# Kernel optimization log

Measured on AMD Instinct MI355X. Metric: run time of the kernel, lower is better.

Reference implementation:

```python
import jax, jax.numpy as jnp
import numpy as np

AXIAL_WEIGHT = 1.0
N_NODES = 1_000_000
N_ELEM = 2_000_000


def setup_inputs() -> dict:
    key = jax.random.key(0)
    ks = jax.random.split(key, 12)
    N, E = N_NODES, N_ELEM
    pred_raw = jax.random.normal(ks[0], (N, 3), jnp.float32)
    u_c = jax.random.uniform(ks[1], (1,), jnp.float32) + 0.5
    theta_c = jax.random.uniform(ks[2], (1,), jnp.float32) + 0.5
    connectivity = jax.random.randint(ks[3], (E, 2), 0, N, jnp.int32)
    # lengths / section properties bounded away from zero (1/L^3 appears)
    elem_lengths = jax.random.uniform(ks[4], (E,), jnp.float32) + 0.5
    prop_E = jax.random.uniform(ks[5], (E,), jnp.float32) + 1.0
    prop_A = jax.random.uniform(ks[6], (E,), jnp.float32) + 0.5
    prop_I22 = jax.random.uniform(ks[7], (E,), jnp.float32) + 0.5
    ang = jax.random.uniform(ks[8], (E,), jnp.float32) * (2.0 * np.pi)
    # columns: [cos, 0, sin] -- forward reads cols 0 and 2
    elem_directions = jnp.stack([jnp.cos(ang), jnp.zeros_like(ang), jnp.sin(ang)], axis=1)
    F_ext = jax.random.normal(ks[9], (N, 3), jnp.float32)
    bc_disp = (jax.random.uniform(ks[10], (N, 1)) < 0.05).astype(jnp.float32)
    bc_rot = (jax.random.uniform(ks[11], (N, 1)) < 0.05).astype(jnp.float32)
    return {
        "pred_raw": pred_raw, "u_c": u_c, "theta_c": theta_c,
        "elem_lengths": elem_lengths, "prop_E": prop_E, "prop_A": prop_A,
        "prop_I22": prop_I22, "elem_directions": elem_directions,
        "F_ext": F_ext, "bc_disp": bc_disp, "bc_rot": bc_rot,
        "connectivity": connectivity,
    }


def reference(pred_raw, u_c, theta_c, elem_lengths, prop_E, prop_A, prop_I22,
              elem_directions, F_ext, bc_disp, bc_rot, connectivity):
    n_nodes = pred_raw.shape[0]
    # physical displacements: [ux*u_c, uz*u_c, th*theta_c]
    scale = jnp.concatenate([u_c, u_c, theta_c])  # [3]
    u_phys = pred_raw * scale[None, :]

    nA = connectivity[:, 0]
    nB = connectivity[:, 1]
    c = elem_directions[:, 0]
    s = elem_directions[:, 2]
    L = elem_lengths
    EA = prop_E * prop_A
    EI = prop_E * prop_I22

    uA = u_phys[nA]  # [E,3] gather
    uB = u_phys[nB]
    u_A = c * uA[:, 0] + s * uA[:, 1]
    w_A = -s * uA[:, 0] + c * uA[:, 1]
    th_A = -uA[:, 2]
    u_B = c * uB[:, 0] + s * uB[:, 1]
    w_B = -s * uB[:, 0] + c * uB[:, 1]
    th_B = -uB[:, 2]

    ea_l = EA / L * AXIAL_WEIGHT
    ei_l = EI / L
    ei_l2 = EI / L**2
    ei_l3 = EI / L**3

    # analytic K_loc @ d_local (K_loc is the standard 6x6 beam stiffness)
    dw = w_A - w_B
    f0 = ea_l * (u_A - u_B)
    f1 = 12.0 * ei_l3 * dw + 6.0 * ei_l2 * (th_A + th_B)
    f2 = 6.0 * ei_l2 * dw + 4.0 * ei_l * th_A + 2.0 * ei_l * th_B
    f3 = -f0
    f4 = -f1
    f5 = 6.0 * ei_l2 * dw + 2.0 * ei_l * th_A + 4.0 * ei_l * th_B

    fA = jnp.stack([c * f0 - s * f1, s * f0 + c * f1, -f2], axis=1)  # [E,3]
    fB = jnp.stack([c * f3 - s * f4, s * f3 + c * f4, -f5], axis=1)

    F_int = jax.ops.segment_sum(
        jnp.concatenate([fA, fB], axis=0),
        jnp.concatenate([nA, nB], axis=0),
        num_segments=n_nodes)  # [N,3] scatter-add

    R = F_int - F_ext
    free_mask = jnp.concatenate([1.0 - bc_disp, 1.0 - bc_disp, 1.0 - bc_rot], axis=1)
    R_free = R * free_mask
    F_free = F_ext * free_mask
    F_norm_sq = jnp.maximum(jnp.sum(F_free**2), 1e-30)
    loss = jnp.sum(R_free**2) / F_norm_sq  # single graph -> n_graphs = 1
    return loss
```

## Files before the change

### kernel.cpp

```cpp
#include <hip/hip_runtime.h>
#include <hip/hip_fp16.h>


#define SPANC  4096
#define NBC    256
#define CURP   16
#define FTH    1024
#define FBE    2048
#define ATH    1024
#define CB     96

struct F3 { float x, y, z; };

__device__ __forceinline__ uint2 packrec(float fx, float fy, float fz, int local) {
    unsigned short hx = __half_as_ushort(__float2half(fx));
    unsigned short hy = __half_as_ushort(__float2half(fy));
    unsigned short hz = __half_as_ushort(__float2half(fz));
    return make_uint2(((unsigned)hy << 16) | hx, ((unsigned)local << 16) | hz);
}

__device__ __forceinline__ int block_incl_scan(int v, int* wsum, int lane, int wv) {
    #pragma unroll
    for (int off = 1; off < 64; off <<= 1) {
        int t = __shfl_up(v, off, 64);
        if (lane >= off) v += t;
    }
    if (lane == 63) wsum[wv] = v;
    __syncthreads();
    if (wv == 0) {
        int w = (lane < 16) ? wsum[lane] : 0;
        #pragma unroll
        for (int off = 1; off < 16; off <<= 1) {
            int t = __shfl_up(w, off, 64);
            if (lane >= off) w += t;
        }
        if (lane < 16) wsum[lane] = w;
    }
    __syncthreads();
    return v + ((wv > 0) ? wsum[wv - 1] : 0);
}

__global__ void __launch_bounds__(1024)
count_kernel(const long long* __restrict__ conn, int* __restrict__ rows,
             int cs, int ce) {
    __shared__ int h[NBC];
    int tid = threadIdx.x;
    if (tid < NBC) h[tid] = 0;
    __syncthreads();
    int stride = gridDim.x * 1024;
    for (int e = cs + blockIdx.x * 1024 + tid; e < ce; e += stride) {
        long long v = __builtin_nontemporal_load(conn + e);
        int na = (int)(unsigned)((unsigned long long)v & 0xFFFFFFFFull);
        int nb = (int)(unsigned)((unsigned long long)v >> 32);
        atomicAdd(&h[na >> 12], 1);
        atomicAdd(&h[nb >> 12], 1);
    }
    __syncthreads();
    if (tid < NBC) rows[blockIdx.x * NBC + tid] = h[tid];
}

__global__ void __launch_bounds__(1024)
scan_kernel(const int* __restrict__ rows, int* __restrict__ cursor,
            int* __restrict__ base, double* __restrict__ accSlots,
            int isFirst) {
    __shared__ int wsum[16];
    int tid = threadIdx.x, lane = tid & 63, wv = tid >> 6;
    int c = 0;
    if (tid < NBC) {
        #pragma unroll 4
        for (int r = 0; r < CB; ++r) c += rows[r * NBC + tid];
    }
    int incl = block_incl_scan(c, wsum, lane, wv);
    if (tid < NBC) {
        base[tid + 1] = incl;
        cursor[tid * CURP] = incl - c;
    }
    if (tid == 0) base[0] = 0;
    if (isFirst && tid < 512) accSlots[tid] = 0.0;
}

__global__ void __launch_bounds__(1024)
fill_kernel(const long long* __restrict__ conn,
            const F3*  __restrict__ pred,
            const float* __restrict__ u_c,
            const float* __restrict__ theta_c,
            const float* __restrict__ len,
            const float* __restrict__ pE,
            const float* __restrict__ pA,
            const float* __restrict__ pI,
            const float* __restrict__ dir,
            uint2* __restrict__ arena,
            int* __restrict__ cursor,
            int cs, int ce) {
    __shared__ uint2         slab[2 * FBE];
    __shared__ unsigned char sbk [2 * FBE];
    __shared__ int hist [NBC];
    __shared__ int boff [NBC];
    __shared__ int astart[NBC];
    __shared__ int wsum [16];

    int tid = threadIdx.x, lane = tid & 63, wv = tid >> 6;

    if (tid < NBC) hist[tid] = 0;
    __syncthreads();

    float uc = u_c[0];
    float tc = theta_c[0];
    int bs = cs + blockIdx.x * FBE;
    int be = bs + FBE; if (be > ce) be = ce;

    unsigned sv[4];
    uint2    rc[4];

    #pragma unroll
    for (int j = 0; j < 2; ++j) {
        int e = bs + j * FTH + tid;
        unsigned sa = 0xFFFFFFFFu, sb = 0xFFFFFFFFu;
        if (e < be) {
            long long cv = __builtin_nontemporal_load(conn + e);
            int na = (int)(unsigned)((unsigned long long)cv & 0xFFFFFFFFull);
            int nb = (int)(unsigned)((unsigned long long)cv >> 32);

            F3 pa_ = pred[na];
            F3 pb_ = pred[nb];

            float c  = __builtin_nontemporal_load(&dir[3 * e + 0]);
            float s  = __builtin_nontemporal_load(&dir[3 * e + 2]);
            float L  = __builtin_nontemporal_load(&len[e]);
            float Ee = __builtin_nontemporal_load(&pE[e]);
            float EA = Ee * __builtin_nontemporal_load(&pA[e]);
            float EI = Ee * __builtin_nontemporal_load(&pI[e]);

            float a0 = pa_.x * uc;
            float a1 = pa_.y * uc;
            float a2 = pa_.z * tc;
            float b0 = pb_.x * uc;
            float b1 = pb_.y * uc;
            float b2 = pb_.z * tc;

            float u_A  =  c * a0 + s * a1;
            float w_A  = -s * a0 + c * a1;
            float th_A = -a2;
            float u_B  =  c * b0 + s * b1;
            float w_B  = -s * b0 + c * b1;
            float th_B = -b2;

            float invL  = 1.0f / L;
            float ea_l  = EA * invL;
            float ei_l  = EI * invL;
            float ei_l2 = ei_l  * invL;
            float ei_l3 = ei_l2 * invL;

            float dw = w_A - w_B;
            float f0 = ea_l * (u_A - u_B);
            float f1 = 12.0f * ei_l3 * dw + 6.0f * ei_l2 * (th_A + th_B);
            float f2 = 6.0f * ei_l2 * dw + 4.0f * ei_l * th_A + 2.0f * ei_l * th_B;
            float f5 = 6.0f * ei_l2 * dw + 2.0f * ei_l * th_A + 4.0f * ei_l * th_B;

            float fA0 = c * f0 - s * f1;
            float fA1 = s * f0 + c * f1;

            int bkA = na >> 12;
            int rA  = atomicAdd(&hist[bkA], 1);
            sa = ((unsigned)rA << 8) | (unsigned)bkA;
            rc[2 * j + 0] = packrec(fA0, fA1, -f2, na & 4095);

            int bkB = nb >> 12;
            int rB  = atomicAdd(&hist[bkB], 1);
            sb = ((unsigned)rB << 8) | (unsigned)bkB;
            rc[2 * j + 1] = packrec(-fA0, -fA1, -f5, nb & 4095);
        }
        sv[2 * j + 0] = sa;
        sv[2 * j + 1] = sb;
    }
    __syncthreads();

    int h = (tid < NBC) ? hist[tid] : 0;
    if (tid < NBC && h) astart[tid] = atomicAdd(&cursor[tid * CURP], h);
    int iT = block_incl_scan(h, wsum, lane, wv);
    if (tid < NBC) boff[tid] = iT - h;
    __syncthreads();

    #pragma unroll
    for (int r = 0; r < 4; ++r) {
        unsigned s2 = sv[r];
        if (s2 != 0xFFFFFFFFu) {
            int bk = (int)(s2 & 255u);
            int rk = (int)(s2 >> 8);
            int slot = boff[bk] + rk;
            slab[slot] = rc[r];
            sbk[slot]  = (unsigned char)bk;
        }
    }
    __syncthreads();

    int tot = boff[NBC - 1] + hist[NBC - 1];
    for (int i = tid; i < tot; i += FTH) {
        int bk = sbk[i];
        arena[astart[bk] + (i - boff[bk])] = slab[i];
    }
}

__global__ void __launch_bounds__(1024)
accum_kernel(const unsigned long long* __restrict__ arena,
             const int* __restrict__ base,
             const float* __restrict__ Fext,
             const float* __restrict__ bcd,
             const float* __restrict__ bcr,
             double* __restrict__ accSlots,
             float* __restrict__ fint32,
             __half* __restrict__ fint16,
             int N, int isFirst, int isLast, int mode) {
    __shared__ float tile[SPANC * 3];
    __shared__ double sn[16], sd[16];

    int tid = threadIdx.x, lane = tid & 63, wv = tid >> 6;
    int b = blockIdx.x;
    int nodeLo = b * SPANC;
    int gBase = nodeLo * 3;
    int gMax  = 3 * N;

    if (isFirst) {
        for (int i = tid; i < SPANC * 3; i += ATH) tile[i] = 0.0f;
    } else if (mode == 1) {
        for (int i = tid; i < SPANC * 3; i += ATH) {
            int g = gBase + i;
            tile[i] = (g < gMax) ? fint32[g] : 0.0f;
        }
    } else {
        for (int i = tid; i < SPANC * 3; i += ATH) {
            int g = gBase + i;
            tile[i] = (g < gMax) ? __half2float(fint16[g]) : 0.0f;
        }
    }
    __syncthreads();

    int s0 = base[b];
    int s1 = base[b + 1];
    for (int i = s0 + tid; i < s1; i += ATH) {
        unsigned long long rv = __builtin_nontemporal_load(arena + i);
        unsigned lo = (unsigned)(rv & 0xFFFFFFFFull);
        unsigned hi = (unsigned)(rv >> 32);
        float fx = __half2float(__ushort_as_half((unsigned short)(lo & 0xFFFFu)));
        float fy = __half2float(__ushort_as_half((unsigned short)(lo >> 16)));
        float fz = __half2float(__ushort_as_half((unsigned short)(hi & 0xFFFFu)));
        int local = (int)(hi >> 16);
        atomicAdd(&tile[local * 3 + 0], fx);
        atomicAdd(&tile[local * 3 + 1], fy);
        atomicAdd(&tile[local * 3 + 2], fz);
    }
    __syncthreads();

    if (!isLast) {
        if (mode == 1) {
            for (int i = tid; i < SPANC * 3; i += ATH) {
                int g = gBase + i;
                if (g < gMax) fint32[g] = tile[i];
            }
        } else {
            for (int i = tid; i < SPANC * 3; i += ATH) {
                int g = gBase + i;
                if (g < gMax) fint16[g] = __float2half(tile[i]);
            }
        }
        return;
    }

    int spanCnt = N - nodeLo;
    if (spanCnt > SPANC) spanCnt = SPANC;

    double num = 0.0, den = 0.0;
    for (int l = tid; l < spanCnt; l += ATH) {
        int n = nodeLo + l;
        float md = 1.0f - __builtin_nontemporal_load(&bcd[n]);
        float mr = 1.0f - __builtin_nontemporal_load(&bcr[n]);
        float e0 = __builtin_nontemporal_load(&Fext[3 * n + 0]);
        float e1 = __builtin_nontemporal_load(&Fext[3 * n + 1]);
        float e2 = __builtin_nontemporal_load(&Fext[3 * n + 2]);
        float r0 = (tile[l * 3 + 0] - e0) * md;
        float r1 = (tile[l * 3 + 1] - e1) * md;
        float r2 = (tile[l * 3 + 2] - e2) * mr;
        float g0 = e0 * md;
        float g1 = e1 * md;
        float g2 = e2 * mr;
        num += (double)r0 * r0 + (double)r1 * r1 + (double)r2 * r2;
        den += (double)g0 * g0 + (double)g1 * g1 + (double)g2 * g2;
    }
    #pragma unroll
    for (int off = 32; off > 0; off >>= 1) {
        num += __shfl_down(num, off, 64);
        den += __shfl_down(den, off, 64);
    }
    if (lane == 0) { sn[wv] = num; sd[wv] = den; }
    __syncthreads();
    if (tid == 0) {
        double tn = 0.0, td = 0.0;
        #pragma unroll
        for (int w = 0; w < 16; ++w) { tn += sn[w]; td += sd[w]; }
        double* slot = accSlots + (size_t)(b & 63) * 8;
        atomicAdd(&slot[0], tn);
        atomicAdd(&slot[1], td);
    }
}

__global__ void final_kernel(const double* __restrict__ accSlots,
                             float* __restrict__ out) {
    int t = threadIdx.x;
    double n = accSlots[t * 8 + 0];
    double d = accSlots[t * 8 + 1];
    #pragma unroll
    for (int off = 32; off > 0; off >>= 1) {
        n += __shfl_down(n, off, 64);
        d += __shfl_down(d, off, 64);
    }
    if (t == 0) {
        if (d < 1e-30) d = 1e-30;
        out[0] = (float)(n / d);
    }
}

static inline size_t align256(size_t x) { return (x + 255) & ~(size_t)255; }

extern "C" void kernel_launch(void* const* d_in, const int* in_sizes, int n_in,
                              void* d_out, int out_size, void* d_ws, size_t ws_size,
                              hipStream_t stream) {
    const F3*    pred    = (const F3*)d_in[0];
    const float* u_c     = (const float*)d_in[1];
    const float* theta_c = (const float*)d_in[2];
    const float* len     = (const float*)d_in[3];
    const float* pE      = (const float*)d_in[4];
    const float* pA      = (const float*)d_in[5];
    const float* pI      = (const float*)d_in[6];
    const float* dir     = (const float*)d_in[7];
    const float* Fext    = (const float*)d_in[8];
    const float* bcd     = (const float*)d_in[9];
    const float* bcr     = (const float*)d_in[10];
    const long long* conn = (const long long*)d_in[11];

    int N = in_sizes[0] / 3;
    int E = in_sizes[3];
    int NBc = (N + SPANC - 1) / SPANC;

    size_t oCur   = 4096;
    size_t oBase  = oCur + (size_t)NBC * CURP * 4;
    size_t oFint0 = align256(oBase + 4 * (NBC + 1));
    size_t rowsBytes = (size_t)CB * NBC * 4;

    const int cfgK[6] = {1, 2, 2, 4, 4, 8};
    const int cfgM[6] = {0, 1, 2, 1, 2, 2};
    int K = 8, mode = 2;
    size_t oF = oFint0, oA = oFint0;
    for (int t = 0; t < 6; ++t) {
        int Kc = cfgK[t], Mc = cfgM[t];
        size_t chunkE = (size_t)(E + Kc - 1) / Kc;
        size_t fsz = (Kc > 1) ? (size_t)3 * N * (Mc == 1 ? 4 : 2) : 0;
        size_t oAt = align256(oFint0 + fsz);
        size_t arenaB = 2 * chunkE * 8;
        if (arenaB < rowsBytes) arenaB = rowsBytes;
        size_t need = oAt + arenaB;
        if (need <= ws_size || t == 5) {
            K = Kc; mode = Mc; oF = oFint0; oA = oAt;
            if (need <= ws_size) break;
        }
    }

    int chunkElems = (E + K - 1) / K;

    double*             accSlots = (double*)d_ws;
    int*                cursor   = (int*)((char*)d_ws + oCur);
    int*                base     = (int*)((char*)d_ws + oBase);
    float*              fint32   = (float*)((char*)d_ws + oF);
    __half*             fint16   = (__half*)((char*)d_ws + oF);
    uint2*              arena    = (uint2*)((char*)d_ws + oA);
    unsigned long long* arenaLL  = (unsigned long long*)arena;
    int*                rows     = (int*)arena;

    for (int c = 0; c < K; ++c) {
        int cs = c * chunkElems;
        if (cs >= E) break;
        int ce = cs + chunkElems;
        if (ce > E) ce = E;
        int NT = (ce - cs + FBE - 1) / FBE;

        int isFirst = (c == 0);
        int isLast  = (ce == E);

        count_kernel<<<CB, 1024, 0, stream>>>(conn, rows, cs, ce);
        scan_kernel<<<1, 1024, 0, stream>>>(rows, cursor, base, accSlots, isFirst);
        fill_kernel<<<NT, FTH, 0, stream>>>(
            conn, pred, u_c, theta_c, len, pE, pA, pI, dir,
            arena, cursor, cs, ce);
        accum_kernel<<<NBc, ATH, 0, stream>>>(
            arenaLL, base, Fext, bcd, bcr, accSlots,
            fint32, fint16, N, isFirst, isLast, mode);
    }

    final_kernel<<<1, 64, 0, stream>>>(accSlots, (float*)d_out);
}
```

Baseline: 278.7 us.

## Prepack scaled node displacements to half, use nontemporal stores, retune chunk configs

```diff
diff --git a/kernel.cpp b/kernel.cpp
--- a/kernel.cpp
+++ b/kernel.cpp
@@ -41,6 +41,21 @@
 }
 
 __global__ void __launch_bounds__(1024)
+upack_kernel(const float* __restrict__ pred, const float* __restrict__ u_c,
+             const float* __restrict__ theta_c, uint2* __restrict__ up, int N) {
+    int i = blockIdx.x * 1024 + threadIdx.x;
+    if (i >= N) return;
+    float uc = u_c[0], tc = theta_c[0];
+    float x = __builtin_nontemporal_load(&pred[3 * i + 0]) * uc;
+    float y = __builtin_nontemporal_load(&pred[3 * i + 1]) * uc;
+    float z = __builtin_nontemporal_load(&pred[3 * i + 2]) * tc;
+    unsigned hx = __half_as_ushort(__float2half(x));
+    unsigned hy = __half_as_ushort(__float2half(y));
+    unsigned hz = __half_as_ushort(__float2half(z));
+    up[i] = make_uint2((hy << 16) | hx, hz);
+}
+
+__global__ void __launch_bounds__(1024)
 count_kernel(const long long* __restrict__ conn, int* __restrict__ rows,
              int cs, int ce) {
     __shared__ int h[NBC];
@@ -56,7 +71,8 @@
         atomicAdd(&h[nb >> 12], 1);
     }
     __syncthreads();
-    if (tid < NBC) rows[blockIdx.x * NBC + tid] = h[tid];
+    if (tid < NBC)
+        __builtin_nontemporal_store(h[tid], &rows[blockIdx.x * NBC + tid]);
 }
 
 __global__ void __launch_bounds__(1024)
@@ -81,9 +97,7 @@
 
 __global__ void __launch_bounds__(1024)
 fill_kernel(const long long* __restrict__ conn,
-            const F3*  __restrict__ pred,
-            const float* __restrict__ u_c,
-            const float* __restrict__ theta_c,
+            const uint2* __restrict__ upk,
             const float* __restrict__ len,
             const float* __restrict__ pE,
             const float* __restrict__ pA,
@@ -104,8 +118,6 @@
     if (tid < NBC) hist[tid] = 0;
     __syncthreads();
 
-    float uc = u_c[0];
-    float tc = theta_c[0];
     int bs = cs + blockIdx.x * FBE;
     int be = bs + FBE; if (be > ce) be = ce;
 
@@ -121,8 +133,8 @@
             int na = (int)(unsigned)((unsigned long long)cv & 0xFFFFFFFFull);
             int nb = (int)(unsigned)((unsigned long long)cv >> 32);
 
-            F3 pa_ = pred[na];
-            F3 pb_ = pred[nb];
+            uint2 ua = upk[na];
+            uint2 ub = upk[nb];
 
             float c  = __builtin_nontemporal_load(&dir[3 * e + 0]);
             float s  = __builtin_nontemporal_load(&dir[3 * e + 2]);
@@ -131,12 +143,12 @@
             float EA = Ee * __builtin_nontemporal_load(&pA[e]);
             float EI = Ee * __builtin_nontemporal_load(&pI[e]);
 
-            float a0 = pa_.x * uc;
-            float a1 = pa_.y * uc;
-            float a2 = pa_.z * tc;
-            float b0 = pb_.x * uc;
-            float b1 = pb_.y * uc;
-            float b2 = pb_.z * tc;
+            float a0 = __half2float(__ushort_as_half((unsigned short)(ua.x & 0xFFFFu)));
+            float a1 = __half2float(__ushort_as_half((unsigned short)(ua.x >> 16)));
+            float a2 = __half2float(__ushort_as_half((unsigned short)(ua.y & 0xFFFFu)));
+            float b0 = __half2float(__ushort_as_half((unsigned short)(ub.x & 0xFFFFu)));
+            float b1 = __half2float(__ushort_as_half((unsigned short)(ub.x >> 16)));
+            float b2 = __half2float(__ushort_as_half((unsigned short)(ub.y & 0xFFFFu)));
 
             float u_A  =  c * a0 + s * a1;
             float w_A  = -s * a0 + c * a1;
@@ -197,7 +209,10 @@
     int tot = boff[NBC - 1] + hist[NBC - 1];
     for (int i = tid; i < tot; i += FTH) {
         int bk = sbk[i];
-        arena[astart[bk] + (i - boff[bk])] = slab[i];
+        uint2 r2 = slab[i];
+        unsigned long long v = ((unsigned long long)r2.y << 32) | (unsigned long long)r2.x;
+        __builtin_nontemporal_store(v,
+            (unsigned long long*)&arena[astart[bk] + (i - boff[bk])]);
     }
 }
 
@@ -209,7 +224,7 @@
              const float* __restrict__ bcr,
              double* __restrict__ accSlots,
              float* __restrict__ fint32,
-             __half* __restrict__ fint16,
+             unsigned short* __restrict__ fint16,
              int N, int isFirst, int isLast, int mode) {
     __shared__ float tile[SPANC * 3];
     __shared__ double sn[16], sd[16];
@@ -225,12 +240,14 @@
     } else if (mode == 1) {
         for (int i = tid; i < SPANC * 3; i += ATH) {
             int g = gBase + i;
-            tile[i] = (g < gMax) ? fint32[g] : 0.0f;
+            tile[i] = (g < gMax) ? __builtin_nontemporal_load(&fint32[g]) : 0.0f;
         }
     } else {
         for (int i = tid; i < SPANC * 3; i += ATH) {
             int g = gBase + i;
-            tile[i] = (g < gMax) ? __half2float(fint16[g]) : 0.0f;
+            tile[i] = (g < gMax)
+                ? __half2float(__ushort_as_half(__builtin_nontemporal_load(&fint16[g])))
+                : 0.0f;
         }
     }
     __syncthreads();
@@ -255,12 +272,14 @@
         if (mode == 1) {
             for (int i = tid; i < SPANC * 3; i += ATH) {
                 int g = gBase + i;
-                if (g < gMax) fint32[g] = tile[i];
+                if (g < gMax) __builtin_nontemporal_store(tile[i], &fint32[g]);
             }
         } else {
             for (int i = tid; i < SPANC * 3; i += ATH) {
                 int g = gBase + i;
-                if (g < gMax) fint16[g] = __float2half(tile[i]);
+                if (g < gMax)
+                    __builtin_nontemporal_store(
+                        __half_as_ushort(__float2half(tile[i])), &fint16[g]);
             }
         }
         return;
@@ -324,7 +343,7 @@
 extern "C" void kernel_launch(void* const* d_in, const int* in_sizes, int n_in,
                               void* d_out, int out_size, void* d_ws, size_t ws_size,
                               hipStream_t stream) {
-    const F3*    pred    = (const F3*)d_in[0];
+    const float* pred    = (const float*)d_in[0];
     const float* u_c     = (const float*)d_in[1];
     const float* theta_c = (const float*)d_in[2];
     const float* len     = (const float*)d_in[3];
@@ -343,11 +362,13 @@
 
     size_t oCur   = 4096;
     size_t oBase  = oCur + (size_t)NBC * CURP * 4;
-    size_t oFint0 = align256(oBase + 4 * (NBC + 1));
+    size_t oU     = align256(oBase + 4 * (NBC + 1));
+    size_t upB    = (size_t)N * 8;
+    size_t oFint0 = align256(oU + upB);
     size_t rowsBytes = (size_t)CB * NBC * 4;
 
-    const int cfgK[6] = {1, 2, 2, 4, 4, 8};
-    const int cfgM[6] = {0, 1, 2, 1, 2, 2};
+    const int cfgK[6] = {1, 2, 3, 4, 6, 8};
+    const int cfgM[6] = {0, 2, 2, 2, 2, 2};
     int K = 8, mode = 2;
     size_t oF = oFint0, oA = oFint0;
     for (int t = 0; t < 6; ++t) {
@@ -369,11 +390,14 @@
     double*             accSlots = (double*)d_ws;
     int*                cursor   = (int*)((char*)d_ws + oCur);
     int*                base     = (int*)((char*)d_ws + oBase);
+    uint2*              upk      = (uint2*)((char*)d_ws + oU);
     float*              fint32   = (float*)((char*)d_ws + oF);
-    __half*             fint16   = (__half*)((char*)d_ws + oF);
+    unsigned short*     fint16   = (unsigned short*)((char*)d_ws + oF);
     uint2*              arena    = (uint2*)((char*)d_ws + oA);
     unsigned long long* arenaLL  = (unsigned long long*)arena;
     int*                rows     = (int*)arena;
+
+    upack_kernel<<<(N + 1023) / 1024, 1024, 0, stream>>>(pred, u_c, theta_c, upk, N);
 
     for (int c = 0; c < K; ++c) {
         int cs = c * chunkElems;
@@ -388,8 +412,7 @@
         count_kernel<<<CB, 1024, 0, stream>>>(conn, rows, cs, ce);
         scan_kernel<<<1, 1024, 0, stream>>>(rows, cursor, base, accSlots, isFirst);
         fill_kernel<<<NT, FTH, 0, stream>>>(
-            conn, pred, u_c, theta_c, len, pE, pA, pI, dir,
-            arena, cursor, cs, ce);
+            conn, upk, len, pE, pA, pI, dir, arena, cursor, cs, ce);
         accum_kernel<<<NBc, ATH, 0, stream>>>(
             arenaLL, base, Fext, bcd, bcr, accSlots,
             fint32, fint16, N, isFirst, isLast, mode);
```

After: 276.3 us. About the same (-0.9%).
